# Performance work log

Measured on AMD Instinct MI355X. Metric: run time of the kernel, lower is better.

Reference implementation:

```python
import jax, jax.numpy as jnp
import numpy as np

N0, N1, N2, N3 = 40000, 10000, 2500, 625
C_IN, C_HID = 64, 256
E0 = N0 * 6
KS = (6, 7, 8)  # KnnEdges(start_k=6, k_increment=1): k = 6 + level
DEPTH = 3


def gcn_conv(x, edge_index, W, b):
    n = x.shape[0]
    loop = jnp.arange(n, dtype=edge_index.dtype)
    src = jnp.concatenate([edge_index[0], loop])
    dst = jnp.concatenate([edge_index[1], loop])
    deg = jax.ops.segment_sum(jnp.ones(src.shape[0], x.dtype), dst, num_segments=n)
    inv = jax.lax.rsqrt(jnp.maximum(deg, 1e-12))
    norm = (inv[src] * inv[dst])[:, None]
    h = x @ W
    return jax.ops.segment_sum(h[src] * norm, dst, num_segments=n) + b


def knn_edges(pos, k):
    # dynamic KNN graph on pooled positions (single graph -> no batch masking)
    n = pos.shape[0]
    sq = jnp.sum(pos * pos, axis=-1)
    d = sq[:, None] + sq[None, :] - 2.0 * (pos @ pos.T)  # [n, n] squared dists
    d = d.at[jnp.arange(n), jnp.arange(n)].set(jnp.inf)  # exclude self
    idx = jax.lax.top_k(-d, k)[1]                        # [n, k] neighbor ids
    src = idx.reshape(-1).astype(jnp.int32)
    dst = jnp.repeat(jnp.arange(n, dtype=jnp.int32), k)
    return jnp.stack([src, dst])


def setup_inputs():
    key = jax.random.key(0)
    ks = jax.random.split(key, 16)
    x = jax.random.normal(ks[0], (N0, C_IN), jnp.float32)
    pos = jax.random.uniform(ks[1], (N0, 2), dtype=jnp.float32)
    edge_index = jax.random.randint(ks[2], (2, E0), 0, N0, jnp.int32)
    # random pooling = randperm prefix (data-independent, precomputed)
    perm1 = jax.random.permutation(ks[3], N0)[:N1].astype(jnp.int32)
    perm2 = jax.random.permutation(ks[4], N1)[:N2].astype(jnp.int32)
    perm3 = jax.random.permutation(ks[5], N2)[:N3].astype(jnp.int32)

    def w(k, i, o):
        return jax.random.normal(k, (i, o), jnp.float32) * (1.0 / np.sqrt(i))

    zb = lambda: jnp.zeros((C_HID,), jnp.float32)
    return dict(
        x=x, pos=pos, edge_index=edge_index,
        perm1=perm1, perm2=perm2, perm3=perm3,
        Wd0=w(ks[6], C_IN, C_HID), bd0=zb(),
        Wd1=w(ks[7], C_HID, C_HID), bd1=zb(),
        Wd2=w(ks[8], C_HID, C_HID), bd2=zb(),
        Wu0=w(ks[9], C_HID, C_HID), bu0=zb(),
        Wu1=w(ks[10], C_HID, C_HID), bu1=zb(),
        Wu2=w(ks[11], C_HID, C_HID), bu2=zb(),
        Wlin=w(ks[12], C_HID, C_HID), blin=zb(),
    )


def reference(x, pos, edge_index, perm1, perm2, perm3,
              Wd0, bd0, Wd1, bd1, Wd2, bd2,
              Wu0, bu0, Wu1, bu1, Wu2, bu2, Wlin, blin):
    down_W, down_b = (Wd0, Wd1, Wd2), (bd0, bd1, bd2)
    up_W, up_b = (Wu0, Wu1, Wu2), (bu0, bu1, bu2)
    perms = (perm1, perm2, perm3)
    edge_indices = [edge_index]
    n_levels = [x.shape[0]]
    # encoder: conv -> relu -> random pool -> dynamic KNN rebuild
    for i in range(DEPTH):
        x = jax.nn.relu(gcn_conv(x, edge_indices[-1], down_W[i], down_b[i]))
        pos = pos[perms[i]]
        edge_indices.append(knn_edges(pos, KS[i]))
        x = x[perms[i]]
        n_levels.append(x.shape[0])
    # decoder: scatter unpool (up[perm] = x) -> conv -> relu
    for i in range(DEPTH):
        up = jnp.zeros((n_levels[-i - 2], x.shape[1]), x.dtype).at[perms[-i - 1]].set(x)
        x = jax.nn.relu(gcn_conv(up, edge_indices[-i - 2], up_W[i], up_b[i]))
    return x @ Wlin + blin
```

## Files before the change

kernel.cpp:

```cpp
#include <hip/hip_runtime.h>
#include <hip/hip_bf16.h>
#include <stdint.h>

#define N0 40000
#define N1 10000
#define N2 2500
#define N3 625
#define E0 240000
#define CIN 64
#define CH 256
#define NBLK ((N0 + 255) / 256)

__global__ void count_deg(const int* __restrict__ dst, int* __restrict__ deg, int e) {
    int i = blockIdx.x * blockDim.x + threadIdx.x;
    if (i < e) atomicAdd(&deg[dst[i]], 1);
}

__global__ __launch_bounds__(256) void scan_blocks(const int* __restrict__ deg,
                                                   int* __restrict__ incl,
                                                   int* __restrict__ bsum, int n) {
    __shared__ int s[256];
    int i = blockIdx.x * 256 + threadIdx.x;
    s[threadIdx.x] = (i < n) ? deg[i] : 0;
    __syncthreads();
#pragma unroll
    for (int off = 1; off < 256; off <<= 1) {
        int t = (threadIdx.x >= off) ? s[threadIdx.x - off] : 0;
        __syncthreads();
        s[threadIdx.x] += t;
        __syncthreads();
    }
    if (i < n) incl[i] = s[threadIdx.x];
    if (threadIdx.x == 255) bsum[blockIdx.x] = s[255];
}

__global__ __launch_bounds__(256) void scan_bsums(int* __restrict__ bsum, int nb) {
    __shared__ int s[256];
    s[threadIdx.x] = (threadIdx.x < nb) ? bsum[threadIdx.x] : 0;
    __syncthreads();
#pragma unroll
    for (int off = 1; off < 256; off <<= 1) {
        int t = (threadIdx.x >= off) ? s[threadIdx.x - off] : 0;
        __syncthreads();
        s[threadIdx.x] += t;
        __syncthreads();
    }
    if (threadIdx.x < nb) bsum[threadIdx.x] = s[threadIdx.x];
}

__global__ void finalize_rowptr(const int* __restrict__ incl, const int* __restrict__ bsum,
                                int* __restrict__ rowptr, int n) {
    int i = blockIdx.x * blockDim.x + threadIdx.x;
    if (i == 0) rowptr[0] = 0;
    if (i < n) {
        int b = i >> 8;
        int off = b ? bsum[b - 1] : 0;
        rowptr[i + 1] = incl[i] + off;
    }
}

__global__ void copy_int(const int* __restrict__ a, int* __restrict__ b, int n) {
    int i = blockIdx.x * blockDim.x + threadIdx.x;
    if (i < n) b[i] = a[i];
}
__global__ void fill_csr(const int* __restrict__ src, const int* __restrict__ dst,
                         int* __restrict__ cursor, int* __restrict__ colsrc, int e) {
    int i = blockIdx.x * blockDim.x + threadIdx.x;
    if (i < e) {
        int d = dst[i];
        int p = atomicAdd(&cursor[d], 1);
        colsrc[p] = src[i];
    }
}
__global__ void make_inv(const int* __restrict__ deg, double* __restrict__ inv, int n) {
    int i = blockIdx.x * blockDim.x + threadIdx.x;
    if (i < n) inv[i] = 1.0 / sqrt((double)(deg[i] + 1));
}

__global__ __launch_bounds__(256) void gemm_f32(
    const float* __restrict__ A, const int* __restrict__ gidx,
    const float* __restrict__ W, const float* __restrict__ bias,
    float* __restrict__ out, int M, int K)
{
    __shared__ float As[16][68];
    __shared__ float Bs[16][132];
    const int tid = threadIdx.x;
    const int tx = tid & 15, ty = tid >> 4;
    const int row0 = blockIdx.x * 64, col0 = blockIdx.y * 128;
    const int sr = tid >> 2;
    const int skq = (tid & 3) * 4;
    const int bkk = tid >> 4;
    const int bc4 = (tid & 15) * 4;
    const int arow = row0 + sr;
    const bool rowok = arow < M;
    long arr = 0;
    if (rowok) arr = (long)(gidx ? gidx[arow] : arow) * K;

    float acc[4][8] = {};
    for (int k0 = 0; k0 < K; k0 += 16) {
        float4 av = make_float4(0.f, 0.f, 0.f, 0.f);
        if (rowok) av = *reinterpret_cast<const float4*>(&A[arr + k0 + skq]);
        As[skq + 0][sr] = av.x;
        As[skq + 1][sr] = av.y;
        As[skq + 2][sr] = av.z;
        As[skq + 3][sr] = av.w;
#pragma unroll
        for (int q = 0; q < 2; ++q) {
            float4 bv = *reinterpret_cast<const float4*>(&W[(long)(k0 + bkk) * CH + col0 + q * 64 + bc4]);
            *reinterpret_cast<float4*>(&Bs[bkk][q * 64 + bc4]) = bv;
        }
        __syncthreads();
#pragma unroll
        for (int kk = 0; kk < 16; ++kk) {
            float4 a4 = *reinterpret_cast<const float4*>(&As[kk][ty * 4]);
            float a[4] = {a4.x, a4.y, a4.z, a4.w};
            float b[8];
#pragma unroll
            for (int q = 0; q < 2; ++q) {
                float4 b4 = *reinterpret_cast<const float4*>(&Bs[kk][q * 64 + tx * 4]);
                b[q * 4 + 0] = b4.x; b[q * 4 + 1] = b4.y;
                b[q * 4 + 2] = b4.z; b[q * 4 + 3] = b4.w;
            }
#pragma unroll
            for (int i = 0; i < 4; i++)
#pragma unroll
                for (int j = 0; j < 8; j++) acc[i][j] += a[i] * b[j];
        }
        __syncthreads();
    }
#pragma unroll
    for (int i = 0; i < 4; i++) {
        int row = row0 + ty * 4 + i;
        if (row >= M) continue;
#pragma unroll
        for (int q = 0; q < 2; ++q) {
            int col = col0 + q * 64 + tx * 4;
            float4 v = make_float4(acc[i][q * 4 + 0], acc[i][q * 4 + 1],
                                   acc[i][q * 4 + 2], acc[i][q * 4 + 3]);
            if (bias) {
                float4 bv = *reinterpret_cast<const float4*>(&bias[col]);
                v.x += bv.x; v.y += bv.y; v.z += bv.z; v.w += bv.w;
            }
            *reinterpret_cast<float4*>(&out[(long)row * CH + col]) = v;
        }
    }
}

__global__ __launch_bounds__(256) void agg_e0(
    const float* __restrict__ h, const int* __restrict__ rowptr,
    const int* __restrict__ colsrc, const double* __restrict__ inv,
    const float* __restrict__ bias, float* __restrict__ out, int n)
{
    __shared__ int s_src[256];
    __shared__ double s_nrm[256];
    int i = blockIdx.x, c = threadIdx.x;
    int r0 = rowptr[i], r1 = rowptr[i + 1];
    double invd = inv[i];
    double acc = (double)h[(long)i * CH + c] * (invd * invd);
    for (int base = r0; base < r1; base += 256) {
        int m = min(256, r1 - base);
        __syncthreads();
        if (c < m) {
            int s = colsrc[base + c];
            s_src[c] = s;
            s_nrm[c] = invd * inv[s];
        }
        __syncthreads();
        for (int j = 0; j < m; ++j)
            acc += (double)h[(long)s_src[j] * CH + c] * s_nrm[j];
    }
    double v = acc + (double)bias[c];
    out[(long)i * CH + c] = (float)fmax(v, 0.0);
}

__global__ void agg_knn(const float* __restrict__ h, const int* __restrict__ idx,
                        const float* __restrict__ b, float* __restrict__ out,
                        int n, int k, double s) {
    int i = blockIdx.x, c = threadIdx.x;
    double acc = (double)h[(long)i * CH + c];
    for (int j = 0; j < k; ++j) {
        int nb = idx[i * k + j];
        acc += (double)h[(long)nb * CH + c];
    }
    double v = acc * s + (double)b[c];
    out[(long)i * CH + c] = (float)fmax(v, 0.0);
}

__global__ void cell_count(const float* __restrict__ pos, int n, int G, int* __restrict__ cnt) {
    int i = blockIdx.x * blockDim.x + threadIdx.x;
    if (i < n) {
        float2 p = ((const float2*)pos)[i];
        int cx = min(G - 1, (int)(p.x * G));
        int cy = min(G - 1, (int)(p.y * G));
        atomicAdd(&cnt[cy * G + cx], 1);
    }
}
__global__ void cell_fill(const float* __restrict__ pos, int n, int G, int* __restrict__ cur,
                          float2* __restrict__ cpos, int* __restrict__ cidx) {
    int i = blockIdx.x * blockDim.x + threadIdx.x;
    if (i < n) {
        float2 p = ((const float2*)pos)[i];
        int cx = min(G - 1, (int)(p.x * G));
        int cy = min(G - 1, (int)(p.y * G));
        int t = atomicAdd(&cur[cy * G + cx], 1);
        cpos[t] = p;
        cidx[t] = i;
    }
}

template <int K>
__global__ void knn_grid(const float* __restrict__ pos, int n, int G,
                         const int* __restrict__ cellptr,
                         const float2* __restrict__ cpos,
                         const int* __restrict__ cidx,
                         int* __restrict__ outIdx) {
    int t0 = blockIdx.x * blockDim.x + threadIdx.x;
    if (t0 >= n) return;
    int q = cidx[t0];
    const float INF = __int_as_float(0x7f800000);
    const float EPS = 1e-5f;
    float h = 1.0f / (float)G;
    float2 qp = cpos[t0];
    float sqq = __fmaf_rn(qp.y, qp.y, __fmul_rn(qp.x, qp.x));
    int cx = min(G - 1, (int)(qp.x * G));
    int cy = min(G - 1, (int)(qp.y * G));
    float bd[K];
    int bi[K];
#pragma unroll
    for (int t = 0; t < K; ++t) { bd[t] = INF; bi[t] = 0x7fffffff; }

    auto visit = [&](int xx, int yy) {
        int ci = yy * G + xx;
        int s = cellptr[ci], e = cellptr[ci + 1];
        for (int t = s; t < e; ++t) {
            float2 pj = cpos[t];
            int j = cidx[t];
            float sqj = __fmaf_rn(pj.y, pj.y, __fmul_rn(pj.x, pj.x));
            float dot = __fmaf_rn(qp.y, pj.y, __fmul_rn(qp.x, pj.x));
            float t1  = __fadd_rn(sqq, sqj);
            float d   = __fmaf_rn(-2.0f, dot, t1);
            if (j == q) continue;
            if (d < bd[K - 1] || (d == bd[K - 1] && j < bi[K - 1])) {
                bd[K - 1] = d; bi[K - 1] = j;
#pragma unroll
                for (int t2 = K - 1; t2 > 0; --t2) {
                    bool sw = (bd[t2] < bd[t2 - 1]) ||
                              (bd[t2] == bd[t2 - 1] && bi[t2] < bi[t2 - 1]);
                    if (sw) {
                        float td = bd[t2]; bd[t2] = bd[t2 - 1]; bd[t2 - 1] = td;
                        int ti = bi[t2]; bi[t2] = bi[t2 - 1]; bi[t2 - 1] = ti;
                    }
                }
            }
        }
    };

    for (int c = 0; c < G; ++c) {
        if (c > 0 && bi[K - 1] != 0x7fffffff) {
            float lim = (float)(c - 1) * h;
            if (lim * lim > bd[K - 1] + EPS) break;
        }
        int y0 = max(0, cy - c), y1 = min(G - 1, cy + c);
        for (int yy = y0; yy <= y1; ++yy) {
            if (yy == cy - c || yy == cy + c) {
                int x0 = max(0, cx - c), x1 = min(G - 1, cx + c);
                for (int xx = x0; xx <= x1; ++xx) visit(xx, yy);
            } else {
                if (cx - c >= 0) visit(cx - c, yy);
                if (cx + c <= G - 1) visit(cx + c, yy);
            }
        }
    }
#pragma unroll
    for (int r = 0; r < K; ++r) outIdx[q * K + r] = bi[r];
}

__global__ void gather_pos(const float* __restrict__ pos, const int* __restrict__ perm,
                           float* __restrict__ out, int m) {
    int i = blockIdx.x * blockDim.x + threadIdx.x;
    if (i < m) {
        int p = perm[i];
        ((float2*)out)[i] = ((const float2*)pos)[p];
    }
}
__global__ void scatter_rows(const float* __restrict__ srcb, const int* __restrict__ perm,
                             float* __restrict__ dst, int m) {
    int i = blockIdx.x, c = threadIdx.x;
    dst[(long)perm[i] * CH + c] = srcb[(long)i * CH + c];
}

extern "C" void kernel_launch(void* const* d_in, const int* in_sizes, int n_in,
                              void* d_out, int out_size, void* d_ws, size_t ws_size,
                              hipStream_t stream) {
    const float* x    = (const float*)d_in[0];
    const float* pos  = (const float*)d_in[1];
    const int*   ei   = (const int*)d_in[2];
    const int*   perm1 = (const int*)d_in[3];
    const int*   perm2 = (const int*)d_in[4];
    const int*   perm3 = (const int*)d_in[5];
    const float* Wd0 = (const float*)d_in[6],  *bd0 = (const float*)d_in[7];
    const float* Wd1 = (const float*)d_in[8],  *bd1 = (const float*)d_in[9];
    const float* Wd2 = (const float*)d_in[10], *bd2 = (const float*)d_in[11];
    const float* Wu0 = (const float*)d_in[12], *bu0 = (const float*)d_in[13];
    const float* Wu1 = (const float*)d_in[14], *bu1 = (const float*)d_in[15];
    const float* Wu2 = (const float*)d_in[16], *bu2 = (const float*)d_in[17];
    const float* Wlin = (const float*)d_in[18], *blin = (const float*)d_in[19];
    float* out = (float*)d_out;

    double* inv0 = (double*)d_ws;
    float* pos1 = (float*)(inv0 + N0);
    float* pos2 = pos1 + N1 * 2;
    float* A   = pos2 + N2 * 2;
    float* C_  = A + (long)N0 * CH;
    float* D_  = C_ + (long)N1 * CH;
    int* degI   = (int*)(D_ + (long)N1 * CH);
    int* rowptr = degI + N0;
    int* cursor = rowptr + N0 + 1;
    int* colsrc = cursor + N0;
    int* idx1   = colsrc + E0;
    int* idx2   = idx1 + N1 * 6;
    int* incl   = idx2 + N2 * 7;
    int* bsum   = incl + N0;
    int* cellcnt = bsum + NBLK;
    int* cellptr = cellcnt + 4096;
    int* ccur    = cellptr + 4097;
    int* cellidx = ccur + 4096;
    float2* cellpos = (float2*)(((uintptr_t)(cellidx + N1) + 15) & ~(uintptr_t)15);
    float* B = out;

    const int* e_src = ei;
    const int* e_dst = ei + E0;

    hipMemsetAsync(degI, 0, (size_t)N0 * sizeof(int), stream);
    count_deg<<<(E0 + 255) / 256, 256, 0, stream>>>(e_dst, degI, E0);
    scan_blocks<<<NBLK, 256, 0, stream>>>(degI, incl, bsum, N0);
    scan_bsums<<<1, 256, 0, stream>>>(bsum, NBLK);
    finalize_rowptr<<<(N0 + 255) / 256, 256, 0, stream>>>(incl, bsum, rowptr, N0);
    copy_int<<<(N0 + 255) / 256, 256, 0, stream>>>(rowptr, cursor, N0);
    fill_csr<<<(E0 + 255) / 256, 256, 0, stream>>>(e_src, e_dst, cursor, colsrc, E0);
    make_inv<<<(N0 + 255) / 256, 256, 0, stream>>>(degI, inv0, N0);

    gemm_f32<<<dim3((N0 + 63) / 64, 2), 256, 0, stream>>>(x, nullptr, Wd0, nullptr, A, N0, CIN);
    agg_e0<<<N0, 256, 0, stream>>>(A, rowptr, colsrc, inv0, bd0, B, N0);

    gather_pos<<<(N1 + 255) / 256, 256, 0, stream>>>(pos, perm1, pos1, N1);
    {
        const int G1 = 64, NC1 = G1 * G1;
        hipMemsetAsync(cellcnt, 0, (size_t)NC1 * sizeof(int), stream);
        cell_count<<<(N1 + 255) / 256, 256, 0, stream>>>(pos1, N1, G1, cellcnt);
        scan_blocks<<<NC1 / 256, 256, 0, stream>>>(cellcnt, incl, bsum, NC1);
        scan_bsums<<<1, 256, 0, stream>>>(bsum, NC1 / 256);
        finalize_rowptr<<<(NC1 + 255) / 256, 256, 0, stream>>>(incl, bsum, cellptr, NC1);
        copy_int<<<(NC1 + 255) / 256, 256, 0, stream>>>(cellptr, ccur, NC1);
        cell_fill<<<(N1 + 255) / 256, 256, 0, stream>>>(pos1, N1, G1, ccur, cellpos, cellidx);
        knn_grid<6><<<(N1 + 255) / 256, 256, 0, stream>>>(pos1, N1, G1, cellptr, cellpos, cellidx, idx1);
    }

    gemm_f32<<<dim3((N1 + 63) / 64, 2), 256, 0, stream>>>(B, perm1, Wd1, nullptr, C_, N1, CH);
    agg_knn<<<N1, 256, 0, stream>>>(C_, idx1, bd1, D_, N1, 6, 1.0 / 7.0);

    gather_pos<<<(N2 + 255) / 256, 256, 0, stream>>>(pos1, perm2, pos2, N2);
    {
        const int G2 = 32, NC2 = G2 * G2;
        hipMemsetAsync(cellcnt, 0, (size_t)NC2 * sizeof(int), stream);
        cell_count<<<(N2 + 255) / 256, 256, 0, stream>>>(pos2, N2, G2, cellcnt);
        scan_blocks<<<NC2 / 256, 256, 0, stream>>>(cellcnt, incl, bsum, NC2);
        scan_bsums<<<1, 256, 0, stream>>>(bsum, NC2 / 256);
        finalize_rowptr<<<(NC2 + 255) / 256, 256, 0, stream>>>(incl, bsum, cellptr, NC2);
        copy_int<<<(NC2 + 255) / 256, 256, 0, stream>>>(cellptr, ccur, NC2);
        cell_fill<<<(N2 + 255) / 256, 256, 0, stream>>>(pos2, N2, G2, ccur, cellpos, cellidx);
        knn_grid<7><<<(N2 + 255) / 256, 256, 0, stream>>>(pos2, N2, G2, cellptr, cellpos, cellidx, idx2);
    }

    gemm_f32<<<dim3((N2 + 63) / 64, 2), 256, 0, stream>>>(D_, perm2, Wd2, nullptr, C_, N2, CH);
    agg_knn<<<N2, 256, 0, stream>>>(C_, idx2, bd2, D_, N2, 7, 1.0 / 8.0);

    gemm_f32<<<dim3((N3 + 63) / 64, 2), 256, 0, stream>>>(D_, perm3, Wu0, nullptr, A, N3, CH);
    hipMemsetAsync(C_, 0, (size_t)N2 * CH * sizeof(float), stream);
    scatter_rows<<<N3, 256, 0, stream>>>(A, perm3, C_, N3);
    agg_knn<<<N2, 256, 0, stream>>>(C_, idx2, bu0, D_, N2, 7, 1.0 / 8.0);

    gemm_f32<<<dim3((N2 + 63) / 64, 2), 256, 0, stream>>>(D_, nullptr, Wu1, nullptr, A, N2, CH);
    hipMemsetAsync(C_, 0, (size_t)N1 * CH * sizeof(float), stream);
    scatter_rows<<<N2, 256, 0, stream>>>(A, perm2, C_, N2);
    agg_knn<<<N1, 256, 0, stream>>>(C_, idx1, bu1, D_, N1, 6, 1.0 / 7.0);

    gemm_f32<<<dim3((N1 + 63) / 64, 2), 256, 0, stream>>>(D_, nullptr, Wu2, nullptr, C_, N1, CH);
    hipMemsetAsync(B, 0, (size_t)N0 * CH * sizeof(float), stream);
    scatter_rows<<<N1, 256, 0, stream>>>(C_, perm1, B, N1);
    agg_e0<<<N0, 256, 0, stream>>>(B, rowptr, colsrc, inv0, bu2, A, N0);

    gemm_f32<<<dim3((N0 + 63) / 64, 2), 256, 0, stream>>>(A, nullptr, Wlin, blin, out, N0, CH);
}
```

Baseline: 640.3 us.

## Double-buffer GEMM shared tiles and fuse cursor copy into rowptr finalize

The fp32 GEMM now keeps two shared-memory tile buffers and prefetches the next K-slice from global memory into registers while the current slice is being computed. This removes one barrier per iteration and hides global load latency. Separately, finalize_rowptr now also writes the cursor array, so three copy_int launches are removed. The cost is doubled LDS use per block, which may reduce occupancy, plus slightly more register pressure.

```diff
diff --git a/kernel.cpp b/kernel.cpp
--- a/kernel.cpp
+++ b/kernel.cpp
@@ -49,20 +49,18 @@
 }
 
 __global__ void finalize_rowptr(const int* __restrict__ incl, const int* __restrict__ bsum,
-                                int* __restrict__ rowptr, int n) {
-    int i = blockIdx.x * blockDim.x + threadIdx.x;
-    if (i == 0) rowptr[0] = 0;
+                                int* __restrict__ rowptr, int* __restrict__ cursor, int n) {
+    int i = blockIdx.x * blockDim.x + threadIdx.x;
+    if (i == 0) { rowptr[0] = 0; cursor[0] = 0; }
     if (i < n) {
         int b = i >> 8;
         int off = b ? bsum[b - 1] : 0;
-        rowptr[i + 1] = incl[i] + off;
-    }
-}
-
-__global__ void copy_int(const int* __restrict__ a, int* __restrict__ b, int n) {
-    int i = blockIdx.x * blockDim.x + threadIdx.x;
-    if (i < n) b[i] = a[i];
-}
+        int v = incl[i] + off;
+        rowptr[i + 1] = v;
+        if (i + 1 < n) cursor[i + 1] = v;
+    }
+}
+
 __global__ void fill_csr(const int* __restrict__ src, const int* __restrict__ dst,
                          int* __restrict__ cursor, int* __restrict__ colsrc, int e) {
     int i = blockIdx.x * blockDim.x + threadIdx.x;
@@ -82,8 +80,8 @@
     const float* __restrict__ W, const float* __restrict__ bias,
     float* __restrict__ out, int M, int K)
 {
-    __shared__ float As[16][68];
-    __shared__ float Bs[16][132];
+    __shared__ float As[2][16][68];
+    __shared__ float Bs[2][16][132];
     const int tid = threadIdx.x;
     const int tx = tid & 15, ty = tid >> 4;
     const int row0 = blockIdx.x * 64, col0 = blockIdx.y * 128;
@@ -96,28 +94,35 @@
     long arr = 0;
     if (rowok) arr = (long)(gidx ? gidx[arow] : arow) * K;
 
+    const int P = K >> 4;
+    float4 av = make_float4(0.f, 0.f, 0.f, 0.f);
+    if (rowok) av = *reinterpret_cast<const float4*>(&A[arr + skq]);
+    float4 bv0 = *reinterpret_cast<const float4*>(&W[(long)bkk * CH + col0 + bc4]);
+    float4 bv1 = *reinterpret_cast<const float4*>(&W[(long)bkk * CH + col0 + 64 + bc4]);
+    As[0][skq + 0][sr] = av.x;  As[0][skq + 1][sr] = av.y;
+    As[0][skq + 2][sr] = av.z;  As[0][skq + 3][sr] = av.w;
+    *reinterpret_cast<float4*>(&Bs[0][bkk][bc4]) = bv0;
+    *reinterpret_cast<float4*>(&Bs[0][bkk][64 + bc4]) = bv1;
+    __syncthreads();
+
     float acc[4][8] = {};
-    for (int k0 = 0; k0 < K; k0 += 16) {
-        float4 av = make_float4(0.f, 0.f, 0.f, 0.f);
-        if (rowok) av = *reinterpret_cast<const float4*>(&A[arr + k0 + skq]);
-        As[skq + 0][sr] = av.x;
-        As[skq + 1][sr] = av.y;
-        As[skq + 2][sr] = av.z;
-        As[skq + 3][sr] = av.w;
-#pragma unroll
-        for (int q = 0; q < 2; ++q) {
-            float4 bv = *reinterpret_cast<const float4*>(&W[(long)(k0 + bkk) * CH + col0 + q * 64 + bc4]);
-            *reinterpret_cast<float4*>(&Bs[bkk][q * 64 + bc4]) = bv;
-        }
-        __syncthreads();
+    for (int p = 0; p < P; ++p) {
+        const int cur = p & 1;
+        if (p + 1 < P) {
+            int k0 = (p + 1) << 4;
+            av = make_float4(0.f, 0.f, 0.f, 0.f);
+            if (rowok) av = *reinterpret_cast<const float4*>(&A[arr + k0 + skq]);
+            bv0 = *reinterpret_cast<const float4*>(&W[(long)(k0 + bkk) * CH + col0 + bc4]);
+            bv1 = *reinterpret_cast<const float4*>(&W[(long)(k0 + bkk) * CH + col0 + 64 + bc4]);
+        }
 #pragma unroll
         for (int kk = 0; kk < 16; ++kk) {
-            float4 a4 = *reinterpret_cast<const float4*>(&As[kk][ty * 4]);
+            float4 a4 = *reinterpret_cast<const float4*>(&As[cur][kk][ty * 4]);
             float a[4] = {a4.x, a4.y, a4.z, a4.w};
             float b[8];
 #pragma unroll
             for (int q = 0; q < 2; ++q) {
-                float4 b4 = *reinterpret_cast<const float4*>(&Bs[kk][q * 64 + tx * 4]);
+                float4 b4 = *reinterpret_cast<const float4*>(&Bs[cur][kk][q * 64 + tx * 4]);
                 b[q * 4 + 0] = b4.x; b[q * 4 + 1] = b4.y;
                 b[q * 4 + 2] = b4.z; b[q * 4 + 3] = b4.w;
             }
@@ -126,7 +131,14 @@
 #pragma unroll
                 for (int j = 0; j < 8; j++) acc[i][j] += a[i] * b[j];
         }
-        __syncthreads();
+        if (p + 1 < P) {
+            const int nxt = cur ^ 1;
+            As[nxt][skq + 0][sr] = av.x;  As[nxt][skq + 1][sr] = av.y;
+            As[nxt][skq + 2][sr] = av.z;  As[nxt][skq + 3][sr] = av.w;
+            *reinterpret_cast<float4*>(&Bs[nxt][bkk][bc4]) = bv0;
+            *reinterpret_cast<float4*>(&Bs[nxt][bkk][64 + bc4]) = bv1;
+            __syncthreads();
+        }
     }
 #pragma unroll
     for (int i = 0; i < 4; i++) {
@@ -335,8 +347,7 @@
     count_deg<<<(E0 + 255) / 256, 256, 0, stream>>>(e_dst, degI, E0);
     scan_blocks<<<NBLK, 256, 0, stream>>>(degI, incl, bsum, N0);
     scan_bsums<<<1, 256, 0, stream>>>(bsum, NBLK);
-    finalize_rowptr<<<(N0 + 255) / 256, 256, 0, stream>>>(incl, bsum, rowptr, N0);
-    copy_int<<<(N0 + 255) / 256, 256, 0, stream>>>(rowptr, cursor, N0);
+    finalize_rowptr<<<(N0 + 255) / 256, 256, 0, stream>>>(incl, bsum, rowptr, cursor, N0);
     fill_csr<<<(E0 + 255) / 256, 256, 0, stream>>>(e_src, e_dst, cursor, colsrc, E0);
     make_inv<<<(N0 + 255) / 256, 256, 0, stream>>>(degI, inv0, N0);
 
@@ -350,8 +361,7 @@
         cell_count<<<(N1 + 255) / 256, 256, 0, stream>>>(pos1, N1, G1, cellcnt);
         scan_blocks<<<NC1 / 256, 256, 0, stream>>>(cellcnt, incl, bsum, NC1);
         scan_bsums<<<1, 256, 0, stream>>>(bsum, NC1 / 256);
-        finalize_rowptr<<<(NC1 + 255) / 256, 256, 0, stream>>>(incl, bsum, cellptr, NC1);
-        copy_int<<<(NC1 + 255) / 256, 256, 0, stream>>>(cellptr, ccur, NC1);
+        finalize_rowptr<<<(NC1 + 255) / 256, 256, 0, stream>>>(incl, bsum, cellptr, ccur, NC1);
         cell_fill<<<(N1 + 255) / 256, 256, 0, stream>>>(pos1, N1, G1, ccur, cellpos, cellidx);
         knn_grid<6><<<(N1 + 255) / 256, 256, 0, stream>>>(pos1, N1, G1, cellptr, cellpos, cellidx, idx1);
     }
@@ -366,8 +376,7 @@
         cell_count<<<(N2 + 255) / 256, 256, 0, stream>>>(pos2, N2, G2, cellcnt);
         scan_blocks<<<NC2 / 256, 256, 0, stream>>>(cellcnt, incl, bsum, NC2);
         scan_bsums<<<1, 256, 0, stream>>>(bsum, NC2 / 256);
-        finalize_rowptr<<<(NC2 + 255) / 256, 256, 0, stream>>>(incl, bsum, cellptr, NC2);
-        copy_int<<<(NC2 + 255) / 256, 256, 0, stream>>>(cellptr, ccur, NC2);
+        finalize_rowptr<<<(NC2 + 255) / 256, 256, 0, stream>>>(incl, bsum, cellptr, ccur, NC2);
         cell_fill<<<(N2 + 255) / 256, 256, 0, stream>>>(pos2, N2, G2, ccur, cellpos, cellidx);
         knn_grid<7><<<(N2 + 255) / 256, 256, 0, stream>>>(pos2, N2, G2, cellptr, cellpos, cellidx, idx2);
     }
```

Measured after the change: 635.5 us. About the same (-0.8%).
